# Optimization experiments

Hardware: AMD Instinct MI355X
Metric: run time of the kernel (lower is better)

The kernel has to match this reference:

```python
import jax, jax.numpy as jnp
import numpy as np

N_U, N_V = 8000, 8000
E_U, E_V = 128000, 128000
ND, ED, T = 40, 10, 3


def _lin(key, out_d, in_d):
    k1, k2 = jax.random.split(key)
    s = 1.0 / np.sqrt(in_d)
    w = jax.random.uniform(k1, (out_d, in_d), minval=-s, maxval=s, dtype=jnp.float32)
    b = jax.random.uniform(k2, (out_d,), minval=-s, maxval=s, dtype=jnp.float32)
    return w, b


def _lstm(key, in_d, h_d):
    ks = jax.random.split(key, 4)
    s = 1.0 / np.sqrt(h_d)
    Wih = jax.random.uniform(ks[0], (4 * h_d, in_d), minval=-s, maxval=s, dtype=jnp.float32)
    Whh = jax.random.uniform(ks[1], (4 * h_d, h_d), minval=-s, maxval=s, dtype=jnp.float32)
    bih = jax.random.uniform(ks[2], (4 * h_d,), minval=-s, maxval=s, dtype=jnp.float32)
    bhh = jax.random.uniform(ks[3], (4 * h_d,), minval=-s, maxval=s, dtype=jnp.float32)
    return Wih, Whh, bih, bhh


def _mp_params(key):
    ks = jax.random.split(key, 2 * T)
    Uw, Ub, Mw, Mb = [], [], [], []
    for k in range(T):
        w, b = _lin(ks[2 * k], ND, 2 * ND + ED); Uw.append(w); Ub.append(b)
        w, b = _lin(ks[2 * k + 1], ND, 2 * ND); Mw.append(w); Mb.append(b)
    return jnp.stack(Uw), jnp.stack(Ub), jnp.stack(Mw), jnp.stack(Mb)


def setup_inputs():
    key = jax.random.key(0)
    ks = jax.random.split(key, 20)
    d = {}
    d["nodes_u"] = jax.random.normal(ks[0], (N_U, ND), jnp.float32)
    d["ei_u"] = jax.random.randint(ks[1], (2, E_U), 0, N_U)
    d["ef_u"] = jax.random.normal(ks[2], (E_U, ED), jnp.float32)
    d["nodes_v"] = jax.random.normal(ks[3], (N_V, ND), jnp.float32)
    d["ei_v"] = jax.random.randint(ks[4], (2, E_V), 0, N_V)
    d["ef_v"] = jax.random.normal(ks[5], (E_V, ED), jnp.float32)
    d["Uw_u"], d["Ub_u"], d["Mw_u"], d["Mb_u"] = _mp_params(ks[6])
    d["Uw_v"], d["Ub_v"], d["Mw_v"], d["Mb_v"] = _mp_params(ks[7])
    d["ls_Wih"], d["ls_Whh"], d["ls_bih"], d["ls_bhh"] = _lstm(ks[8], 2 * ND, ND)
    d["lv_Wih"], d["lv_Whh"], d["lv_bih"], d["lv_bhh"] = _lstm(ks[9], 2 * ND, ND)
    d["gs_Wih"], d["gs_Whh"], d["gs_bih"], d["gs_bhh"] = _lstm(ks[10], 8 * ND, 4 * ND)
    d["gv_Wih"], d["gv_Whh"], d["gv_bih"], d["gv_bhh"] = _lstm(ks[11], 8 * ND, 4 * ND)
    d["w1"], d["b1"] = _lin(ks[12], 360, 16 * ND)
    d["w2"], d["b2"] = _lin(ks[13], 200, 360)
    d["w3"], d["b3"] = _lin(ks[14], 120, 200)
    d["w4"], d["b4"] = _lin(ks[15], 1, 120)
    return d


def _lstm_step(x, h, c, Wih, Whh, bih, bhh):
    # one seq_len=1 step of torch nn.LSTM; gate order i, f, g, o
    gates = x @ Wih.T + h @ Whh.T + bih + bhh
    i, f, g, o = jnp.split(gates, 4, axis=-1)
    c = jax.nn.sigmoid(f) * c + jax.nn.sigmoid(i) * jnp.tanh(g)
    h = jax.nn.sigmoid(o) * jnp.tanh(c)
    return h, c


def _message_passing(h, ei, ef, Uw, Ub, Mw, Mb):
    # vectorized form of the per-node Python loop: messages use the
    # pre-update h each round (the torch code computes all messages first).
    src, dst = ei[0], ei[1]
    n = h.shape[0]
    for k in range(T):
        z = jnp.concatenate([h[src], h[dst], ef], axis=-1)   # [E, 2*ND+ED]
        msg_e = z @ Uw[k].T + Ub[k]                          # [E, ND]
        msg = jax.ops.segment_sum(msg_e, src, num_segments=n)
        h = jax.nn.relu(jnp.concatenate([h, msg], axis=-1) @ Mw[k].T + Mb[k])
    return h


def _set2set_pair(h0, ht, Wih, Whh, bih, bhh, steps=2):
    # set of size 2 ({h_0, h_T}) per node; nodes act as the LSTM batch.
    t = jnp.stack([h0, ht], axis=0)                # [2, n, f]
    n, f = h0.shape
    q_star = jnp.zeros((n, 2 * f), h0.dtype)
    h = jnp.zeros((n, f), h0.dtype)
    c = jnp.zeros((n, f), h0.dtype)
    for _ in range(steps):
        h, c = _lstm_step(q_star, h, c, Wih, Whh, bih, bhh)
        e = jnp.sum(t * h[None], axis=2)           # [2, n]
        a = jax.nn.softmax(e, axis=0)
        r = jnp.sum(a[..., None] * t, axis=0)      # [n, f]
        q_star = jnp.concatenate([h, r], axis=1)
    return q_star                                   # [n, 2f]


def _set2set_pool(x, Wih, Whh, bih, bhh, steps=2):
    # attention pooling over nodes, batch of 1 (the gather set2set).
    n, f = x.shape
    q_star = jnp.zeros((1, 2 * f), x.dtype)
    h = jnp.zeros((1, f), x.dtype)
    c = jnp.zeros((1, f), x.dtype)
    for _ in range(steps):
        h, c = _lstm_step(q_star, h, c, Wih, Whh, bih, bhh)
        a = jax.nn.softmax(x @ h[0])                # [n]
        r = (a[:, None] * x).sum(axis=0, keepdims=True)
        q_star = jnp.concatenate([h, r], axis=1)
    return q_star                                    # [1, 2f]


def reference(nodes_u, ei_u, ef_u, nodes_v, ei_v, ef_v,
              Uw_u, Ub_u, Mw_u, Mb_u, Uw_v, Ub_v, Mw_v, Mb_v,
              ls_Wih, ls_Whh, ls_bih, ls_bhh,
              lv_Wih, lv_Whh, lv_bih, lv_bhh,
              gs_Wih, gs_Whh, gs_bih, gs_bhh,
              gv_Wih, gv_Whh, gv_bih, gv_bhh,
              w1, b1, w2, b2, w3, b3, w4, b4):
    hu_t = _message_passing(nodes_u, ei_u, ef_u, Uw_u, Ub_u, Mw_u, Mb_u)
    hv_t = _message_passing(nodes_v, ei_v, ef_v, Uw_v, Ub_v, Mw_v, Mb_v)
    gu = _set2set_pair(nodes_u, hu_t, ls_Wih, ls_Whh, ls_bih, ls_bhh)  # [n, 2*ND]
    gv = _set2set_pair(nodes_v, hv_t, lv_Wih, lv_Whh, lv_bih, lv_bhh)  # [m, 2*ND]
    interaction = gu @ gv.T                          # [n, m]
    im2 = jnp.tanh(interaction)
    u_after = im2 @ gv                               # [n, 2*ND]
    v_after = im2.T @ gu                             # [m, 2*ND]
    cu = _set2set_pool(jnp.concatenate([u_after, gu], 1), gs_Wih, gs_Whh, gs_bih, gs_bhh)
    cv = _set2set_pool(jnp.concatenate([v_after, gv], 1), gv_Wih, gv_Whh, gv_bih, gv_bhh)
    x = jnp.concatenate([cu, cv], axis=1)            # [1, 16*ND]
    x = jax.nn.relu(x @ w1.T + b1)
    x = jax.nn.relu(x @ w2.T + b2)
    x = jax.nn.relu(x @ w3.T + b3)
    x = x @ w4.T + b4                                # [1, 1]
    return (x, interaction)
```

## Files before the change

kernel.cpp:

```cpp
#include <hip/hip_runtime.h>
#include <cstdint>
#include <cstddef>

#define NN 8000
#define NE 128000
#define NDv 40
#define EDv 10

typedef __attribute__((ext_vector_type(8))) short short8v;
typedef __attribute__((ext_vector_type(4))) float f32x4;

__device__ __forceinline__ float rcp_fast(float x) { return __builtin_amdgcn_rcpf(x); }
__device__ __forceinline__ float sigm(float x) { return rcp_fast(1.f + __expf(-x)); }
__device__ __forceinline__ float ftanh(float x) {
    float e = __expf(2.f * x);
    return 1.f - 2.f * rcp_fast(e + 1.f);
}
__device__ __forceinline__ short f2bf(float x) {
    unsigned u = __builtin_bit_cast(unsigned, x);
    u += 0x7fffu + ((u >> 16) & 1u);
    return (short)(u >> 16);
}
__device__ __forceinline__ float wsum(float v) {
    for (int o = 32; o; o >>= 1) v += __shfl_down(v, o);
    return v;
}
__device__ __forceinline__ float wmax(float v) {
    for (int o = 32; o; o >>= 1) v = fmaxf(v, __shfl_down(v, o));
    return v;
}


__global__ __launch_bounds__(256) void csr_deg2_kernel(const int* __restrict__ ei_u, const int* __restrict__ ei_v,
                                                       int* __restrict__ deg_u, int* __restrict__ deg_v) {
    const int* ei = blockIdx.y ? ei_v : ei_u;
    int* deg = blockIdx.y ? deg_v : deg_u;
    int e = blockIdx.x * 256 + threadIdx.x;
    if (e < NE) atomicAdd(&deg[ei[e]], 1);
}

__global__ __launch_bounds__(256) void sef2_kernel(const int* __restrict__ ei_u, const int* __restrict__ ei_v,
                                                   const float* __restrict__ ef_u, const float* __restrict__ ef_v,
                                                   float* __restrict__ sef_u, float* __restrict__ sef_v) {
    const int* ei = blockIdx.y ? ei_v : ei_u;
    const float* ef = blockIdx.y ? ef_v : ef_u;
    float* sef = blockIdx.y ? sef_v : sef_u;
    int t = blockIdx.x * 256 + threadIdx.x;
    int e = t / EDv, k = t % EDv;
    atomicAdd(&sef[ei[e] * EDv + k], ef[t]);
}

__global__ __launch_bounds__(64) void csr_scan2_kernel(const int* __restrict__ deg_u, const int* __restrict__ deg_v,
                                                       int* __restrict__ off_u, int* __restrict__ off_v,
                                                       int* __restrict__ woff_u, int* __restrict__ woff_v) {
    const int* deg = blockIdx.x ? deg_v : deg_u;
    int* off = blockIdx.x ? off_v : off_u;
    int* woff = blockIdx.x ? woff_v : woff_u;
    int l = threadIdx.x;
    int base = l * 125;
    int s = 0;
    for (int i = 0; i < 125; ++i) s += deg[base + i];
    int pre = s;
    for (int o = 1; o < 64; o <<= 1) { int t = __shfl_up(pre, o); if (l >= o) pre += t; }
    pre -= s;
    int run = pre;
    for (int i = 0; i < 125; ++i) {
        off[base + i] = run; woff[base + i] = run;
        run += deg[base + i];
    }
    if (l == 63) off[NN] = run;
}

__global__ __launch_bounds__(256) void csr_fill2_kernel(const int* __restrict__ ei_u, const int* __restrict__ ei_v,
                                                        int* __restrict__ woff_u, int* __restrict__ woff_v,
                                                        int* __restrict__ dl_u, int* __restrict__ dl_v) {
    const int* ei = blockIdx.y ? ei_v : ei_u;
    int* woff = blockIdx.y ? woff_v : woff_u;
    int* dlist = blockIdx.y ? dl_v : dl_u;
    int e = blockIdx.x * 256 + threadIdx.x;
    if (e < NE) { int p = atomicAdd(&woff[ei[e]], 1); dlist[p] = ei[NE + e]; }
}


__global__ __launch_bounds__(256) void node_proj2_kernel(const float* __restrict__ h_u, const float* __restrict__ h_v,
                                                         const float* __restrict__ Uw_u, const float* __restrict__ Uw_v,
                                                         float* __restrict__ A_u, float* __restrict__ B_u,
                                                         float* __restrict__ A_v, float* __restrict__ B_v) {
    const float* h = blockIdx.y ? h_v : h_u;
    const float* Uw = blockIdx.y ? Uw_v : Uw_u;
    float* A = blockIdx.y ? A_v : A_u;
    float* B = blockIdx.y ? B_v : B_u;
    __shared__ float W[40][81];
    int tid = threadIdx.x;
    for (int s = tid; s < 3200; s += 256) W[s / 80][s % 80] = Uw[(s / 80) * 90 + (s % 80)];
    __syncthreads();
    int t = blockIdx.x * 256 + tid;
    int n = t / NDv, i = t % NDv;
    float hreg[40];
    const float* hr = h + n * NDv;
#pragma unroll
    for (int k4 = 0; k4 < 10; ++k4) {
        float4 v = *reinterpret_cast<const float4*>(hr + k4 * 4);
        hreg[k4 * 4 + 0] = v.x; hreg[k4 * 4 + 1] = v.y; hreg[k4 * 4 + 2] = v.z; hreg[k4 * 4 + 3] = v.w;
    }
    float a = 0.f, b = 0.f;
#pragma unroll
    for (int k = 0; k < NDv; ++k) { a += W[i][k] * hreg[k]; b += W[i][40 + k] * hreg[k]; }
    A[t] = a; B[t] = b;
}

__global__ __launch_bounds__(320) void mp_round2_kernel(
    const int* __restrict__ off_u, const int* __restrict__ dl_u, const float* __restrict__ sef_u,
    const float* __restrict__ UwE_u, const float* __restrict__ Ub_u,
    const float* __restrict__ Mw_u, const float* __restrict__ Mb_u, const float* __restrict__ UwN_u,
    const float* __restrict__ h_u, const float* __restrict__ A_u, const float* __restrict__ B_u,
    float* __restrict__ hout_u, float* __restrict__ Ao_u, float* __restrict__ Bo_u,
    const int* __restrict__ off_v, const int* __restrict__ dl_v, const float* __restrict__ sef_v,
    const float* __restrict__ UwE_v, const float* __restrict__ Ub_v,
    const float* __restrict__ Mw_v, const float* __restrict__ Mb_v, const float* __restrict__ UwN_v,
    const float* __restrict__ h_v, const float* __restrict__ A_v, const float* __restrict__ B_v,
    float* __restrict__ hout_v, float* __restrict__ Ao_v, float* __restrict__ Bo_v,
    int has_next) {
    const int* off = blockIdx.y ? off_v : off_u;
    const int* dlist = blockIdx.y ? dl_v : dl_u;
    const float* sef = blockIdx.y ? sef_v : sef_u;
    const float* UwE = blockIdx.y ? UwE_v : UwE_u;
    const float* Ub = blockIdx.y ? Ub_v : Ub_u;
    const float* Mw = blockIdx.y ? Mw_v : Mw_u;
    const float* Mb = blockIdx.y ? Mb_v : Mb_u;
    const float* UwN = blockIdx.y ? UwN_v : UwN_u;
    const float* h = blockIdx.y ? h_v : h_u;
    const float* A = blockIdx.y ? A_v : A_u;
    const float* B = blockIdx.y ? B_v : B_u;
    float* hout = blockIdx.y ? hout_v : hout_u;
    float* Ao = blockIdx.y ? Ao_v : Ao_u;
    float* Bo = blockIdx.y ? Bo_v : Bo_u;

    __shared__ float WM[40][81];
    __shared__ float WU[40][81];
    __shared__ float msgS[8][40];
    __shared__ float hS[8][41];
    __shared__ float houtS[8][41];

    int tid = threadIdx.x;
    for (int s = tid; s < 3200; s += 320) WM[s / 80][s % 80] = Mw[s];
    if (has_next)
        for (int s = tid; s < 3200; s += 320) WU[s / 80][s % 80] = UwN[(s / 80) * 90 + (s % 80)];
    int ln = tid / NDv, i = tid % NDv;
    int n = blockIdx.x * 8 + ln;
    int t = n * NDv + i;
    hS[ln][i] = h[t];

    const float* we = UwE + i * 90 + 80;
    const float* se = sef + n * EDv;
    int p0 = off[n], p1 = off[n + 1];
    float acc = (float)(p1 - p0) * (A[t] + Ub[i]);
#pragma unroll
    for (int k = 0; k < EDv; ++k) acc += we[k] * se[k];
    for (int p = p0; p < p1; ++p) acc += B[dlist[p] * NDv + i];
    msgS[ln][i] = acc;
    __syncthreads();

    float a2 = Mb[i];
#pragma unroll
    for (int k = 0; k < NDv; ++k) a2 += WM[i][k] * hS[ln][k];
#pragma unroll
    for (int k = 0; k < NDv; ++k) a2 += WM[i][40 + k] * msgS[ln][k];
    float ho = fmaxf(a2, 0.f);
    hout[t] = ho;
    if (has_next) {
        houtS[ln][i] = ho;
        __syncthreads();
        float a = 0.f, b = 0.f;
#pragma unroll
        for (int k = 0; k < NDv; ++k) { float hv = houtS[ln][k]; a += WU[i][k] * hv; b += WU[i][40 + k] * hv; }
        Ao[t] = a; Bo[t] = b;
    }
}


__global__ __launch_bounds__(64) void s2s_init2_kernel(const float* __restrict__ bih_u, const float* __restrict__ bhh_u,
                                                       const float* __restrict__ bih_v, const float* __restrict__ bhh_v,
                                                       float* __restrict__ h1_u, float* __restrict__ c1_u,
                                                       float* __restrict__ h1_v, float* __restrict__ c1_v) {
    const float* bih = blockIdx.y ? bih_v : bih_u;
    const float* bhh = blockIdx.y ? bhh_v : bhh_u;
    float* h1 = blockIdx.y ? h1_v : h1_u;
    float* c1 = blockIdx.y ? c1_v : c1_u;
    int i = threadIdx.x;
    if (i < 40) {
        float gi = bih[i] + bhh[i];
        float gf = bih[40 + i] + bhh[40 + i];
        (void)gf;
        float gg = bih[80 + i] + bhh[80 + i];
        float go = bih[120 + i] + bhh[120 + i];
        float c = sigm(gi) * ftanh(gg);
        c1[i] = c;
        h1[i] = sigm(go) * ftanh(c);
    }
}

__global__ __launch_bounds__(256) void s2s_step0_kernel(const float* __restrict__ h0_u, const float* __restrict__ ht_u,
                                                        const float* __restrict__ h1_u, float* __restrict__ q_u,
                                                        const float* __restrict__ h0_v, const float* __restrict__ ht_v,
                                                        const float* __restrict__ h1_v, float* __restrict__ q_v) {
    const float* h0 = blockIdx.y ? h0_v : h0_u;
    const float* ht = blockIdx.y ? ht_v : ht_u;
    const float* h1 = blockIdx.y ? h1_v : h1_u;
    float* q = blockIdx.y ? q_v : q_u;
    int tid = threadIdx.x;
    int nl = tid >> 2, lg = tid & 3;
    int n = blockIdx.x * 64 + nl;
    float h0r[10], htr[10];
    float e0 = 0.f, e1 = 0.f;
#pragma unroll
    for (int k = 0; k < 10; ++k) {
        int i = lg * 10 + k;
        h0r[k] = h0[n * 40 + i];
        htr[k] = ht[n * 40 + i];
        float hv = h1[i];
        e0 += h0r[k] * hv;
        e1 += htr[k] * hv;
    }
    e0 += __shfl_xor(e0, 1); e0 += __shfl_xor(e0, 2);
    e1 += __shfl_xor(e1, 1); e1 += __shfl_xor(e1, 2);
    float m = fmaxf(e0, e1);
    float p0 = __expf(e0 - m), p1 = __expf(e1 - m);
    float inv = rcp_fast(p0 + p1);
    float a0 = p0 * inv, a1 = p1 * inv;
#pragma unroll
    for (int k = 0; k < 10; ++k) {
        int i = lg * 10 + k;
        q[n * 80 + i] = h1[i];
        q[n * 80 + 40 + i] = a0 * h0r[k] + a1 * htr[k];
    }
}

__global__ __launch_bounds__(64) void s2s_base2_kernel(const float* __restrict__ Wih_u, const float* __restrict__ Whh_u,
                                                       const float* __restrict__ bih_u, const float* __restrict__ bhh_u,
                                                       const float* __restrict__ h1_u,
                                                       const float* __restrict__ Wih_v, const float* __restrict__ Whh_v,
                                                       const float* __restrict__ bih_v, const float* __restrict__ bhh_v,
                                                       const float* __restrict__ h1_v,
                                                       float* __restrict__ base2) {
    const float* Wih = blockIdx.y ? Wih_v : Wih_u;
    const float* Whh = blockIdx.y ? Whh_v : Whh_u;
    const float* bih = blockIdx.y ? bih_v : bih_u;
    const float* bhh = blockIdx.y ? bhh_v : bhh_u;
    const float* h1 = blockIdx.y ? h1_v : h1_u;
    int j = blockIdx.x;
    int lane = threadIdx.x;
    float p = 0.f;
    if (lane < 40) p = (Wih[j * 80 + lane] + Whh[j * 40 + lane]) * h1[lane];
    p = wsum(p);
    if (lane == 0) base2[blockIdx.y * 160 + j] = p + bih[j] + bhh[j];
}

__global__ __launch_bounds__(256) void s2s_gates1_kernel(const float* __restrict__ q_u, const float* __restrict__ Wih_u,
                                                         float* __restrict__ gT_u,
                                                         const float* __restrict__ q_v, const float* __restrict__ Wih_v,
                                                         float* __restrict__ gT_v,
                                                         const float* __restrict__ base2) {
    const float* q = blockIdx.y ? q_v : q_u;
    const float* Wih = blockIdx.y ? Wih_v : Wih_u;
    float* gatesT = blockIdx.y ? gT_v : gT_u;
    const float* base = base2 + blockIdx.y * 160;
    int t = blockIdx.x * 256 + threadIdx.x;
    int n = t % NN;
    int jg = t / NN;
    float rr[40];
#pragma unroll
    for (int k4 = 0; k4 < 10; ++k4) {
        float4 v = *reinterpret_cast<const float4*>(q + n * 80 + 40 + k4 * 4);
        rr[k4 * 4 + 0] = v.x; rr[k4 * 4 + 1] = v.y; rr[k4 * 4 + 2] = v.z; rr[k4 * 4 + 3] = v.w;
    }
#pragma unroll
    for (int jj = 0; jj < 8; ++jj) {
        int j = jg * 8 + jj;
        const float* wi = Wih + j * 80 + 40;
        float acc = base[j];
#pragma unroll
        for (int k = 0; k < 40; ++k) acc += wi[k] * rr[k];
        gatesT[j * NN + n] = acc;
    }
}

__global__ __launch_bounds__(256) void s2s_upd1_kernel(const float* __restrict__ gT_u, const float* __restrict__ h0_u,
                                                       const float* __restrict__ ht_u, const float* __restrict__ c1_u,
                                                       float* __restrict__ q_u,
                                                       const float* __restrict__ gT_v, const float* __restrict__ h0_v,
                                                       const float* __restrict__ ht_v, const float* __restrict__ c1_v,
                                                       float* __restrict__ q_v) {
    const float* gT = blockIdx.y ? gT_v : gT_u;
    const float* h0 = blockIdx.y ? h0_v : h0_u;
    const float* ht = blockIdx.y ? ht_v : ht_u;
    const float* c1 = blockIdx.y ? c1_v : c1_u;
    float* q = blockIdx.y ? q_v : q_u;
    int tid = threadIdx.x;
    int nl = tid >> 2, lg = tid & 3;
    int n = blockIdx.x * 64 + nl;
    float h0r[10], htr[10], hnr[10];
    float e0 = 0.f, e1 = 0.f;
#pragma unroll
    for (int k = 0; k < 10; ++k) {
        int i = lg * 10 + k;
        float gi = gT[i * NN + n];
        float gf = gT[(40 + i) * NN + n];
        float gg = gT[(80 + i) * NN + n];
        float go = gT[(120 + i) * NN + n];
        float cn = sigm(gf) * c1[i] + sigm(gi) * ftanh(gg);
        float hn = sigm(go) * ftanh(cn);
        hnr[k] = hn;
        h0r[k] = h0[n * 40 + i];
        htr[k] = ht[n * 40 + i];
        e0 += h0r[k] * hn;
        e1 += htr[k] * hn;
    }
    e0 += __shfl_xor(e0, 1); e0 += __shfl_xor(e0, 2);
    e1 += __shfl_xor(e1, 1); e1 += __shfl_xor(e1, 2);
    float m = fmaxf(e0, e1);
    float p0 = __expf(e0 - m), p1 = __expf(e1 - m);
    float inv = rcp_fast(p0 + p1);
    float a0 = p0 * inv, a1 = p1 * inv;
#pragma unroll
    for (int k = 0; k < 10; ++k) {
        int i = lg * 10 + k;
        q[n * 80 + i] = hnr[k];
        q[n * 80 + 40 + i] = a0 * h0r[k] + a1 * htr[k];
    }
}


__global__ __launch_bounds__(256) void cast_all_kernel(const float* __restrict__ gu, const float* __restrict__ gv,
                                                       short* __restrict__ ouT, short* __restrict__ ovT,
                                                       short* __restrict__ oub, short* __restrict__ ovb) {
    const float* g = blockIdx.y ? gv : gu;
    if (blockIdx.x < 2500) {
        short* o = blockIdx.y ? ovT : ouT;
        int t = blockIdx.x * 256 + threadIdx.x;
        int m = t % NN, f = t / NN;
        o[t] = f2bf(g[m * 80 + f]);
    } else {
        short* o = blockIdx.y ? ovb : oub;
        int t = (blockIdx.x - 2500) * 256 + threadIdx.x;
        int m = t / 96, k = t % 96;
        o[t] = (k < 80) ? f2bf(g[m * 80 + k]) : (short)0;
    }
}


__global__ __launch_bounds__(256, 2) void fused_kernel(const short* __restrict__ gub, const short* __restrict__ gvb,
                                                       const short* __restrict__ guT, const short* __restrict__ gvT,
                                                       float* __restrict__ inter,
                                                       float* __restrict__ uafT, float* __restrict__ vafT) {
    __shared__ short P[4][16][72];
    const short* Xb; const short* Yb; const short* YT; float* afT;
    bool storeI = (blockIdx.z == 0);
    if (storeI) { Xb = gub; Yb = gvb; YT = gvT; afT = uafT; }
    else        { Xb = gvb; Yb = gub; YT = guT; afT = vafT; }
    int tid = threadIdx.x;
    int w = tid >> 6, l = tid & 63;
    int lrow = l & 15, lk = l >> 4;
    int x0 = blockIdx.x * 64;
    int it0 = (125 * blockIdx.y) >> 3;
    int it1 = (125 * (blockIdx.y + 1)) >> 3;
    short8v a_x[3];
    const short* arow = Xb + (size_t)(x0 + w * 16 + lrow) * 96 + lk * 8;
#pragma unroll
    for (int ks = 0; ks < 3; ++ks) a_x[ks] = *reinterpret_cast<const short8v*>(arow + ks * 32);
    const short* ybase = Yb + (size_t)lrow * 96 + lk * 8;

    f32x4 acc[5] = {};
    short8v bc[12], bn[12];
#pragma unroll
    for (int i = 0; i < 12; ++i) {
        int ks = i >> 2, nt = i & 3;
        bc[i] = *reinterpret_cast<const short8v*>(ybase + (size_t)(it0 * 64 + nt * 16) * 96 + ks * 32);
    }
    for (int it = it0; it < it1; ++it) {
        int k0 = it * 64;
        if (it + 1 < it1) {
#pragma unroll
            for (int i = 0; i < 12; ++i) {
                int ks = i >> 2, nt = i & 3;
                bn[i] = *reinterpret_cast<const short8v*>(ybase + (size_t)(k0 + 64 + nt * 16) * 96 + ks * 32);
            }
        }
        short8v byt[10];
#pragma unroll
        for (int ks2 = 0; ks2 < 2; ++ks2)
#pragma unroll
            for (int ft = 0; ft < 5; ++ft)
                byt[ks2 * 5 + ft] = *reinterpret_cast<const short8v*>(YT + (size_t)(ft * 16 + lrow) * NN + k0 + ks2 * 32 + lk * 8);
        f32x4 accI[4] = {};
#pragma unroll
        for (int ks = 0; ks < 3; ++ks)
#pragma unroll
            for (int nt = 0; nt < 4; ++nt)
                accI[nt] = __builtin_amdgcn_mfma_f32_16x16x32_bf16(a_x[ks], bc[ks * 4 + nt], accI[nt], 0, 0, 0);
#pragma unroll
        for (int nt = 0; nt < 4; ++nt)
#pragma unroll
            for (int r = 0; r < 4; ++r)
                P[w][lk * 4 + r][nt * 16 + lrow] = f2bf(ftanh(accI[nt][r]));
#pragma unroll
        for (int ks2 = 0; ks2 < 2; ++ks2) {
            short8v ap = *reinterpret_cast<const short8v*>(&P[w][lrow][ks2 * 32 + lk * 8]);
#pragma unroll
            for (int ft = 0; ft < 5; ++ft)
                acc[ft] = __builtin_amdgcn_mfma_f32_16x16x32_bf16(ap, byt[ks2 * 5 + ft], acc[ft], 0, 0, 0);
        }
        if (storeI) {
#pragma unroll
            for (int nt = 0; nt < 4; ++nt)
#pragma unroll
                for (int r = 0; r < 4; ++r)
                    inter[(size_t)(x0 + w * 16 + lk * 4 + r) * NN + (k0 + nt * 16 + lrow)] = accI[nt][r];
        }
#pragma unroll
        for (int i = 0; i < 12; ++i) bc[i] = bn[i];
    }
    int xout = x0 + w * 16 + lk * 4;
#pragma unroll
    for (int ft = 0; ft < 5; ++ft)
#pragma unroll
        for (int r = 0; r < 4; ++r)
            atomicAdd(&afT[(size_t)(ft * 16 + lrow) * NN + xout + r], acc[ft][r]);
}


__global__ __launch_bounds__(64) void gates_pool2_kernel(const float* __restrict__ Wih_u, const float* __restrict__ Whh_u,
                                                         const float* __restrict__ bih_u, const float* __restrict__ bhh_u,
                                                         const float* __restrict__ q_u, const float* __restrict__ h_u,
                                                         const float* __restrict__ Wih_v, const float* __restrict__ Whh_v,
                                                         const float* __restrict__ bih_v, const float* __restrict__ bhh_v,
                                                         const float* __restrict__ q_v, const float* __restrict__ h_v,
                                                         float* __restrict__ gts2) {
    const float* Wih = blockIdx.y ? Wih_v : Wih_u;
    const float* Whh = blockIdx.y ? Whh_v : Whh_u;
    const float* bih = blockIdx.y ? bih_v : bih_u;
    const float* bhh = blockIdx.y ? bhh_v : bhh_u;
    const float* q = blockIdx.y ? q_v : q_u;
    const float* h = blockIdx.y ? h_v : h_u;
    float* gts = gts2 + blockIdx.y * 640;
    int j = blockIdx.x;
    int lane = threadIdx.x;
    const float* wi = Wih + j * 320;
    const float* wh = Whh + j * 160;
    float p = 0.f;
#pragma unroll
    for (int k4 = 0; k4 < 5; ++k4) { int k = lane + k4 * 64; p += wi[k] * q[k]; }
#pragma unroll
    for (int k4 = 0; k4 < 3; ++k4) { int k = lane + k4 * 64; if (k < 160) p += wh[k] * h[k]; }
    p = wsum(p);
    if (lane == 0) gts[j] = p + bih[j] + bhh[j];
}

__global__ __launch_bounds__(256) void pool_point2_kernel(const float* __restrict__ gts2,
                                                          float* __restrict__ h_u, float* __restrict__ c_u,
                                                          float* __restrict__ q_u,
                                                          float* __restrict__ h_v, float* __restrict__ c_v,
                                                          float* __restrict__ q_v) {
    const float* gts = gts2 + blockIdx.y * 640;
    float* h = blockIdx.y ? h_v : h_u;
    float* c = blockIdx.y ? c_v : c_u;
    float* q = blockIdx.y ? q_v : q_u;
    int tid = threadIdx.x;
    if (tid < 160) {
        float cn = sigm(gts[160 + tid]) * c[tid] + sigm(gts[tid]) * ftanh(gts[320 + tid]);
        c[tid] = cn;
        float hn = sigm(gts[480 + tid]) * ftanh(cn);
        h[tid] = hn;
        q[tid] = hn;
    }
}

__global__ __launch_bounds__(256) void pool_scores2_kernel(const float* __restrict__ uafT, const float* __restrict__ g_u,
                                                           const float* __restrict__ h_u, float* __restrict__ sc_u,
                                                           const float* __restrict__ vafT, const float* __restrict__ g_v,
                                                           const float* __restrict__ h_v, float* __restrict__ sc_v,
                                                           float* __restrict__ pmax2) {
    const float* afT = blockIdx.y ? vafT : uafT;
    const float* g = blockIdx.y ? g_v : g_u;
    const float* h = blockIdx.y ? h_v : h_u;
    float* scores = blockIdx.y ? sc_v : sc_u;
    float* pmax = pmax2 + blockIdx.y * 32;
    int tid = threadIdx.x;
    int n = blockIdx.x * 256 + tid;
    float s = -3.4e38f;
    if (n < NN) {
        float acc = 0.f;
#pragma unroll 8
        for (int k = 0; k < 80; ++k) acc += afT[k * NN + n] * h[k];
        const float* gr = g + n * 80;
#pragma unroll 8
        for (int k = 0; k < 80; ++k) acc += gr[k] * h[80 + k];
        scores[n] = acc;
        s = acc;
    }
    __shared__ float red[4];
    float m = wmax(s);
    if ((tid & 63) == 0) red[tid >> 6] = m;
    __syncthreads();
    if (tid == 0) pmax[blockIdx.x] = fmaxf(fmaxf(red[0], red[1]), fmaxf(red[2], red[3]));
}

__global__ __launch_bounds__(256) void pool_r2_kernel(const float* __restrict__ uafT, const float* __restrict__ g_u,
                                                      const float* __restrict__ sc_u,
                                                      const float* __restrict__ vafT, const float* __restrict__ g_v,
                                                      const float* __restrict__ sc_v,
                                                      const float* __restrict__ pmax2,
                                                      float* __restrict__ pq_u, float* __restrict__ pq_v) {
    const float* afT = blockIdx.y ? vafT : uafT;
    const float* g = blockIdx.y ? g_v : g_u;
    const float* scores = blockIdx.y ? sc_v : sc_u;
    float* q = blockIdx.y ? pq_v : pq_u;
    const float* pmax = pmax2 + blockIdx.y * 32;
    int f = blockIdx.x;
    int tid = threadIdx.x;
    __shared__ float smax;
    __shared__ float reda[4], redd[4];
    if (tid < 64) {
        float m = (tid < 32) ? pmax[tid] : -3.4e38f;
        m = wmax(m);
        if (tid == 0) smax = m;
    }
    __syncthreads();
    float m = smax;
    float acc = 0.f, den = 0.f;
    if (f < 80) {
        const float* x = afT + (size_t)f * NN;
        for (int n = tid; n < NN; n += 256) { float e = __expf(scores[n] - m); den += e; acc += e * x[n]; }
    } else {
        const float* x = g + (f - 80);
        for (int n = tid; n < NN; n += 256) { float e = __expf(scores[n] - m); den += e; acc += e * x[(size_t)n * 80]; }
    }
    float wa = wsum(acc), wd = wsum(den);
    if ((tid & 63) == 0) { reda[tid >> 6] = wa; redd[tid >> 6] = wd; }
    __syncthreads();
    if (tid == 0) {
        float A = reda[0] + reda[1] + reda[2] + reda[3];
        float D = redd[0] + redd[1] + redd[2] + redd[3];
        q[160 + f] = A * rcp_fast(D);
    }
}


__global__ __launch_bounds__(64) void gemv_kernel(const float* __restrict__ W, const float* __restrict__ b,
                                                  const float* __restrict__ x, float* __restrict__ y,
                                                  int K, int relu) {
    int j = blockIdx.x;
    int lane = threadIdx.x;
    const float* w = W + (size_t)j * K;
    float p = 0.f;
    for (int k = lane; k < K; k += 64) p += w[k] * x[k];
    p = wsum(p);
    if (lane == 0) {
        p += b[j];
        y[j] = relu ? fmaxf(p, 0.f) : p;
    }
}


extern "C" void kernel_launch(void* const* d_in, const int* in_sizes, int n_in,
                              void* d_out, int out_size, void* d_ws, size_t ws_size,
                              hipStream_t stream) {
    const float* nodes_u = (const float*)d_in[0];
    const int* ei_u = (const int*)d_in[1];
    const float* ef_u = (const float*)d_in[2];
    const float* nodes_v = (const float*)d_in[3];
    const int* ei_v = (const int*)d_in[4];
    const float* ef_v = (const float*)d_in[5];
    const float* Uw_u = (const float*)d_in[6];
    const float* Ub_u = (const float*)d_in[7];
    const float* Mw_u = (const float*)d_in[8];
    const float* Mb_u = (const float*)d_in[9];
    const float* Uw_v = (const float*)d_in[10];
    const float* Ub_v = (const float*)d_in[11];
    const float* Mw_v = (const float*)d_in[12];
    const float* Mb_v = (const float*)d_in[13];
    const float* lsWih = (const float*)d_in[14];
    const float* lsWhh = (const float*)d_in[15];
    const float* lsbih = (const float*)d_in[16];
    const float* lsbhh = (const float*)d_in[17];
    const float* lvWih = (const float*)d_in[18];
    const float* lvWhh = (const float*)d_in[19];
    const float* lvbih = (const float*)d_in[20];
    const float* lvbhh = (const float*)d_in[21];
    const float* gsWih = (const float*)d_in[22];
    const float* gsWhh = (const float*)d_in[23];
    const float* gsbih = (const float*)d_in[24];
    const float* gsbhh = (const float*)d_in[25];
    const float* gvWih = (const float*)d_in[26];
    const float* gvWhh = (const float*)d_in[27];
    const float* gvbih = (const float*)d_in[28];
    const float* gvbhh = (const float*)d_in[29];
    const float* w1 = (const float*)d_in[30];
    const float* b1 = (const float*)d_in[31];
    const float* w2 = (const float*)d_in[32];
    const float* b2 = (const float*)d_in[33];
    const float* w3 = (const float*)d_in[34];
    const float* b3 = (const float*)d_in[35];
    const float* w4 = (const float*)d_in[36];
    const float* b4 = (const float*)d_in[37];

    float* ws = (float*)d_ws;
    float* hA_u = ws + 0;
    float* hB_u = ws + 320000;
    float* hA_v = ws + 640000;
    float* hB_v = ws + 960000;
    float* A0_u = ws + 1600000;
    float* B0_u = ws + 1920000;
    float* q_u  = ws + 2240000;
    float* q_v  = ws + 2880000;
    float* A1_u = ws + 2240000;
    float* B1_u = ws + 2560000;
    float* A1_v = ws + 2880000;
    float* B1_v = ws + 3200000;
    float* sef_u = ws + 4160000;
    float* sef_v = ws + 4240000;
    float* gT_u = ws + 4160000;
    float* gT_v = ws + 5440000;
    float* uafT = ws + 5440000;
    float* vafT = ws + 6080000;
    float* sc_u = ws + 6720000;
    float* sc_v = ws + 6728000;
    float* pmax2 = ws + 6736000;
    float* pq_u = ws + 6736080;
    float* pq_v = ws + 6736400;
    float* ph_u = ws + 6736720;
    float* pc_u = ws + 6736880;
    float* ph_v = ws + 6737040;
    float* pc_v = ws + 6737200;
    float* pgts2 = ws + 6737360;
    float* mx1  = ws + 6738640;
    float* mx2  = ws + 6739000;
    float* mx3  = ws + 6739200;
    float* h1_u = ws + 6739320;
    float* c1_u = ws + 6739360;
    float* h1_v = ws + 6739400;
    float* c1_v = ws + 6739440;
    float* base2 = ws + 6739480;
    int* ioff_u   = (int*)(ws + 6740000);
    int* idlist_u = (int*)(ws + 6748064);
    int* ioff_v   = (int*)(ws + 6876064);
    int* idlist_v = (int*)(ws + 6884128);
    int* iwoff_u  = (int*)(ws + 7012128);
    int* ideg_u   = (int*)(ws + 7020192);
    int* iwoff_v  = (int*)(ws + 7028256);
    int* ideg_v   = (int*)(ws + 7036320);
    float* A0_v = ws + 7339536;
    float* B0_v = ws + 7659536;

    short* guT = (short*)(ws + 0);
    short* gvT = (short*)(ws + 320000);
    short* gub = (short*)(ws + 640000);
    short* gvb = (short*)(ws + 1024000);

    float* out = (float*)d_out;
    float* inter = out + 1;

    hipMemsetAsync(ideg_u, 0, (7044384 - 7020192) * sizeof(int), stream);
    hipMemsetAsync(sef_u, 0, 2 * NN * EDv * sizeof(float), stream);
    csr_deg2_kernel<<<dim3(500, 2), 256, 0, stream>>>(ei_u, ei_v, ideg_u, ideg_v);
    csr_scan2_kernel<<<2, 64, 0, stream>>>(ideg_u, ideg_v, ioff_u, ioff_v, iwoff_u, iwoff_v);
    csr_fill2_kernel<<<dim3(500, 2), 256, 0, stream>>>(ei_u, ei_v, iwoff_u, iwoff_v, idlist_u, idlist_v);
    sef2_kernel<<<dim3(5000, 2), 256, 0, stream>>>(ei_u, ei_v, ef_u, ef_v, sef_u, sef_v);

    node_proj2_kernel<<<dim3(1250, 2), 256, 0, stream>>>(nodes_u, nodes_v, Uw_u, Uw_v, A0_u, B0_u, A0_v, B0_v);
    mp_round2_kernel<<<dim3(1000, 2), 320, 0, stream>>>(
        ioff_u, idlist_u, sef_u, Uw_u, Ub_u, Mw_u, Mb_u, Uw_u + 3600,
        nodes_u, A0_u, B0_u, hA_u, A1_u, B1_u,
        ioff_v, idlist_v, sef_v, Uw_v, Ub_v, Mw_v, Mb_v, Uw_v + 3600,
        nodes_v, A0_v, B0_v, hA_v, A1_v, B1_v, 1);
    mp_round2_kernel<<<dim3(1000, 2), 320, 0, stream>>>(
        ioff_u, idlist_u, sef_u, Uw_u + 3600, Ub_u + 40, Mw_u + 3200, Mb_u + 40, Uw_u + 7200,
        hA_u, A1_u, B1_u, hB_u, A0_u, B0_u,
        ioff_v, idlist_v, sef_v, Uw_v + 3600, Ub_v + 40, Mw_v + 3200, Mb_v + 40, Uw_v + 7200,
        hA_v, A1_v, B1_v, hB_v, A0_v, B0_v, 1);
    mp_round2_kernel<<<dim3(1000, 2), 320, 0, stream>>>(
        ioff_u, idlist_u, sef_u, Uw_u + 7200, Ub_u + 80, Mw_u + 6400, Mb_u + 80, nullptr,
        hB_u, A0_u, B0_u, hA_u, nullptr, nullptr,
        ioff_v, idlist_v, sef_v, Uw_v + 7200, Ub_v + 80, Mw_v + 6400, Mb_v + 80, nullptr,
        hB_v, A0_v, B0_v, hA_v, nullptr, nullptr, 0);

    s2s_init2_kernel<<<dim3(1, 2), 64, 0, stream>>>(lsbih, lsbhh, lvbih, lvbhh, h1_u, c1_u, h1_v, c1_v);
    s2s_step0_kernel<<<dim3(125, 2), 256, 0, stream>>>(nodes_u, hA_u, h1_u, q_u, nodes_v, hA_v, h1_v, q_v);
    s2s_base2_kernel<<<dim3(160, 2), 64, 0, stream>>>(lsWih, lsWhh, lsbih, lsbhh, h1_u,
                                                      lvWih, lvWhh, lvbih, lvbhh, h1_v, base2);
    s2s_gates1_kernel<<<dim3(625, 2), 256, 0, stream>>>(q_u, lsWih, gT_u, q_v, lvWih, gT_v, base2);
    s2s_upd1_kernel<<<dim3(125, 2), 256, 0, stream>>>(gT_u, nodes_u, hA_u, c1_u, q_u,
                                                      gT_v, nodes_v, hA_v, c1_v, q_v);

    cast_all_kernel<<<dim3(5500, 2), 256, 0, stream>>>(q_u, q_v, guT, gvT, gub, gvb);

    hipMemsetAsync(uafT, 0, 1280000 * sizeof(float), stream);
    fused_kernel<<<dim3(125, 8, 2), 256, 0, stream>>>(gub, gvb, guT, gvT, inter, uafT, vafT);

    hipMemsetAsync(pq_u, 0, 1280 * sizeof(float), stream);
    for (int stp = 0; stp < 2; ++stp) {
        gates_pool2_kernel<<<dim3(640, 2), 64, 0, stream>>>(gsWih, gsWhh, gsbih, gsbhh, pq_u, ph_u,
                                                            gvWih, gvWhh, gvbih, gvbhh, pq_v, ph_v, pgts2);
        pool_point2_kernel<<<dim3(1, 2), 256, 0, stream>>>(pgts2, ph_u, pc_u, pq_u, ph_v, pc_v, pq_v);
        pool_scores2_kernel<<<dim3(32, 2), 256, 0, stream>>>(uafT, q_u, ph_u, sc_u, vafT, q_v, ph_v, sc_v, pmax2);
        pool_r2_kernel<<<dim3(160, 2), 256, 0, stream>>>(uafT, q_u, sc_u, vafT, q_v, sc_v, pmax2, pq_u, pq_v);
    }

    gemv_kernel<<<360, 64, 0, stream>>>(w1, b1, pq_u, mx1, 640, 1);
    gemv_kernel<<<200, 64, 0, stream>>>(w2, b2, mx1, mx2, 360, 1);
    gemv_kernel<<<120, 64, 0, stream>>>(w3, b3, mx2, mx3, 200, 1);
    gemv_kernel<<<1, 64, 0, stream>>>(w4, b4, mx3, out, 120, 0);
}
```

Baseline: 690.7 us.

## Transpose pooled features, split fused kernel in four, specialize first pool step

The cast kernel also writes an fp32 transposed copy of the node features. The pooling scores and readout kernels now read these with coalesced, feature-major loads instead of strided row access. The fused interaction kernel now splits the column range into 4 chunks instead of 8, which halves the atomic accumulation traffic but gives fewer blocks. The first set2set pooling step starts from zero state, so its gates reduce to the biases; a tiny init kernel computes them and replaces one full gates GEMV pass.

```diff
diff --git a/kernel.cpp b/kernel.cpp
--- a/kernel.cpp
+++ b/kernel.cpp
@@ -190,8 +190,6 @@
     int i = threadIdx.x;
     if (i < 40) {
         float gi = bih[i] + bhh[i];
-        float gf = bih[40 + i] + bhh[40 + i];
-        (void)gf;
         float gg = bih[80 + i] + bhh[80 + i];
         float go = bih[120 + i] + bhh[120 + i];
         float c = sigm(gi) * ftanh(gg);
@@ -333,13 +331,17 @@
 
 __global__ __launch_bounds__(256) void cast_all_kernel(const float* __restrict__ gu, const float* __restrict__ gv,
                                                        short* __restrict__ ouT, short* __restrict__ ovT,
-                                                       short* __restrict__ oub, short* __restrict__ ovb) {
+                                                       short* __restrict__ oub, short* __restrict__ ovb,
+                                                       float* __restrict__ qTu, float* __restrict__ qTv) {
     const float* g = blockIdx.y ? gv : gu;
     if (blockIdx.x < 2500) {
         short* o = blockIdx.y ? ovT : ouT;
+        float* qT = blockIdx.y ? qTv : qTu;
         int t = blockIdx.x * 256 + threadIdx.x;
         int m = t % NN, f = t / NN;
-        o[t] = f2bf(g[m * 80 + f]);
+        float val = g[m * 80 + f];
+        o[t] = f2bf(val);
+        qT[t] = val;
     } else {
         short* o = blockIdx.y ? ovb : oub;
         int t = (blockIdx.x - 2500) * 256 + threadIdx.x;
@@ -362,8 +364,8 @@
     int w = tid >> 6, l = tid & 63;
     int lrow = l & 15, lk = l >> 4;
     int x0 = blockIdx.x * 64;
-    int it0 = (125 * blockIdx.y) >> 3;
-    int it1 = (125 * (blockIdx.y + 1)) >> 3;
+    int it0 = (125 * blockIdx.y) >> 2;
+    int it1 = (125 * (blockIdx.y + 1)) >> 2;
     short8v a_x[3];
     const short* arow = Xb + (size_t)(x0 + w * 16 + lrow) * 96 + lk * 8;
 #pragma unroll
@@ -428,6 +430,30 @@
             atomicAdd(&afT[(size_t)(ft * 16 + lrow) * NN + xout + r], acc[ft][r]);
 }
 
+
+__global__ __launch_bounds__(256) void pool_init2_kernel(const float* __restrict__ bih_u, const float* __restrict__ bhh_u,
+                                                         const float* __restrict__ bih_v, const float* __restrict__ bhh_v,
+                                                         float* __restrict__ ph_u, float* __restrict__ pc_u,
+                                                         float* __restrict__ pq_u,
+                                                         float* __restrict__ ph_v, float* __restrict__ pc_v,
+                                                         float* __restrict__ pq_v) {
+    const float* bih = blockIdx.y ? bih_v : bih_u;
+    const float* bhh = blockIdx.y ? bhh_v : bhh_u;
+    float* ph = blockIdx.y ? ph_v : ph_u;
+    float* pc = blockIdx.y ? pc_v : pc_u;
+    float* pq = blockIdx.y ? pq_v : pq_u;
+    int i = threadIdx.x;
+    if (i < 160) {
+        float gi = bih[i] + bhh[i];
+        float gg = bih[320 + i] + bhh[320 + i];
+        float go = bih[480 + i] + bhh[480 + i];
+        float c = sigm(gi) * ftanh(gg);
+        pc[i] = c;
+        float h = sigm(go) * ftanh(c);
+        ph[i] = h;
+        pq[i] = h;
+    }
+}
 
 __global__ __launch_bounds__(64) void gates_pool2_kernel(const float* __restrict__ Wih_u, const float* __restrict__ Whh_u,
                                                          const float* __restrict__ bih_u, const float* __restrict__ bhh_u,
@@ -475,13 +501,13 @@
     }
 }
 
-__global__ __launch_bounds__(256) void pool_scores2_kernel(const float* __restrict__ uafT, const float* __restrict__ g_u,
+__global__ __launch_bounds__(256) void pool_scores2_kernel(const float* __restrict__ uafT, const float* __restrict__ qTu,
                                                            const float* __restrict__ h_u, float* __restrict__ sc_u,
-                                                           const float* __restrict__ vafT, const float* __restrict__ g_v,
+                                                           const float* __restrict__ vafT, const float* __restrict__ qTv,
                                                            const float* __restrict__ h_v, float* __restrict__ sc_v,
                                                            float* __restrict__ pmax2) {
     const float* afT = blockIdx.y ? vafT : uafT;
-    const float* g = blockIdx.y ? g_v : g_u;
+    const float* qT = blockIdx.y ? qTv : qTu;
     const float* h = blockIdx.y ? h_v : h_u;
     float* scores = blockIdx.y ? sc_v : sc_u;
     float* pmax = pmax2 + blockIdx.y * 32;
@@ -492,9 +518,8 @@
         float acc = 0.f;
 #pragma unroll 8
         for (int k = 0; k < 80; ++k) acc += afT[k * NN + n] * h[k];
-        const float* gr = g + n * 80;
 #pragma unroll 8
-        for (int k = 0; k < 80; ++k) acc += gr[k] * h[80 + k];
+        for (int k = 0; k < 80; ++k) acc += qT[k * NN + n] * h[80 + k];
         scores[n] = acc;
         s = acc;
     }
@@ -505,14 +530,14 @@
     if (tid == 0) pmax[blockIdx.x] = fmaxf(fmaxf(red[0], red[1]), fmaxf(red[2], red[3]));
 }
 
-__global__ __launch_bounds__(256) void pool_r2_kernel(const float* __restrict__ uafT, const float* __restrict__ g_u,
+__global__ __launch_bounds__(256) void pool_r2_kernel(const float* __restrict__ uafT, const float* __restrict__ qTu,
                                                       const float* __restrict__ sc_u,
-                                                      const float* __restrict__ vafT, const float* __restrict__ g_v,
+                                                      const float* __restrict__ vafT, const float* __restrict__ qTv,
                                                       const float* __restrict__ sc_v,
                                                       const float* __restrict__ pmax2,
                                                       float* __restrict__ pq_u, float* __restrict__ pq_v) {
     const float* afT = blockIdx.y ? vafT : uafT;
-    const float* g = blockIdx.y ? g_v : g_u;
+    const float* qT = blockIdx.y ? qTv : qTu;
     const float* scores = blockIdx.y ? sc_v : sc_u;
     float* q = blockIdx.y ? pq_v : pq_u;
     const float* pmax = pmax2 + blockIdx.y * 32;
@@ -527,14 +552,9 @@
     }
     __syncthreads();
     float m = smax;
+    const float* x = (f < 80) ? (afT + (size_t)f * NN) : (qT + (size_t)(f - 80) * NN);
     float acc = 0.f, den = 0.f;
-    if (f < 80) {
-        const float* x = afT + (size_t)f * NN;
-        for (int n = tid; n < NN; n += 256) { float e = __expf(scores[n] - m); den += e; acc += e * x[n]; }
-    } else {
-        const float* x = g + (f - 80);
-        for (int n = tid; n < NN; n += 256) { float e = __expf(scores[n] - m); den += e; acc += e * x[(size_t)n * 80]; }
-    }
+    for (int n = tid; n < NN; n += 256) { float e = __expf(scores[n] - m); den += e; acc += e * x[n]; }
     float wa = wsum(acc), wd = wsum(den);
     if ((tid & 63) == 0) { reda[tid >> 6] = wa; redd[tid >> 6] = wd; }
     __syncthreads();
@@ -623,6 +643,8 @@
     float* gT_v = ws + 5440000;
     float* uafT = ws + 5440000;
     float* vafT = ws + 6080000;
+    float* qT_u = ws + 1600000;
+    float* qT_v = ws + 1920000;
     float* sc_u = ws + 6720000;
     float* sc_v = ws + 6728000;
     float* pmax2 = ws + 6736000;
@@ -692,19 +714,20 @@
     s2s_upd1_kernel<<<dim3(125, 2), 256, 0, stream>>>(gT_u, nodes_u, hA_u, c1_u, q_u,
                                                       gT_v, nodes_v, hA_v, c1_v, q_v);
 
-    cast_all_kernel<<<dim3(5500, 2), 256, 0, stream>>>(q_u, q_v, guT, gvT, gub, gvb);
+    cast_all_kernel<<<dim3(5500, 2), 256, 0, stream>>>(q_u, q_v, guT, gvT, gub, gvb, qT_u, qT_v);
 
     hipMemsetAsync(uafT, 0, 1280000 * sizeof(float), stream);
-    fused_kernel<<<dim3(125, 8, 2), 256, 0, stream>>>(gub, gvb, guT, gvT, inter, uafT, vafT);
-
-    hipMemsetAsync(pq_u, 0, 1280 * sizeof(float), stream);
-    for (int stp = 0; stp < 2; ++stp) {
-        gates_pool2_kernel<<<dim3(640, 2), 64, 0, stream>>>(gsWih, gsWhh, gsbih, gsbhh, pq_u, ph_u,
-                                                            gvWih, gvWhh, gvbih, gvbhh, pq_v, ph_v, pgts2);
-        pool_point2_kernel<<<dim3(1, 2), 256, 0, stream>>>(pgts2, ph_u, pc_u, pq_u, ph_v, pc_v, pq_v);
-        pool_scores2_kernel<<<dim3(32, 2), 256, 0, stream>>>(uafT, q_u, ph_u, sc_u, vafT, q_v, ph_v, sc_v, pmax2);
-        pool_r2_kernel<<<dim3(160, 2), 256, 0, stream>>>(uafT, q_u, sc_u, vafT, q_v, sc_v, pmax2, pq_u, pq_v);
-    }
+    fused_kernel<<<dim3(125, 4, 2), 256, 0, stream>>>(gub, gvb, guT, gvT, inter, uafT, vafT);
+
+    pool_init2_kernel<<<dim3(1, 2), 256, 0, stream>>>(gsbih, gsbhh, gvbih, gvbhh,
+                                                      ph_u, pc_u, pq_u, ph_v, pc_v, pq_v);
+    pool_scores2_kernel<<<dim3(32, 2), 256, 0, stream>>>(uafT, qT_u, ph_u, sc_u, vafT, qT_v, ph_v, sc_v, pmax2);
+    pool_r2_kernel<<<dim3(160, 2), 256, 0, stream>>>(uafT, qT_u, sc_u, vafT, qT_v, sc_v, pmax2, pq_u, pq_v);
+    gates_pool2_kernel<<<dim3(640, 2), 64, 0, stream>>>(gsWih, gsWhh, gsbih, gsbhh, pq_u, ph_u,
+                                                        gvWih, gvWhh, gvbih, gvbhh, pq_v, ph_v, pgts2);
+    pool_point2_kernel<<<dim3(1, 2), 256, 0, stream>>>(pgts2, ph_u, pc_u, pq_u, ph_v, pc_v, pq_v);
+    pool_scores2_kernel<<<dim3(32, 2), 256, 0, stream>>>(uafT, qT_u, ph_u, sc_u, vafT, qT_v, ph_v, sc_v, pmax2);
+    pool_r2_kernel<<<dim3(160, 2), 256, 0, stream>>>(uafT, qT_u, sc_u, vafT, qT_v, sc_v, pmax2, pq_u, pq_v);
 
     gemv_kernel<<<360, 64, 0, stream>>>(w1, b1, pq_u, mx1, 640, 1);
     gemv_kernel<<<200, 64, 0, stream>>>(w2, b2, mx1, mx2, 360, 1);
```

Result: faster. 654.4 us (-5.3%).
